# Kernel optimization log

Measured on AMD Instinct MI355X. Metric: run time of the kernel, lower is better.

The kernel has to match this reference:

```python
import jax, jax.numpy as jnp
import numpy as np

B, T, C, H = 4, 2048, 1024, 16
D = C // H  # head_dim = 64


def setup_inputs() -> dict:
    key = jax.random.key(0)
    k1, k2, k3, k4, k5 = jax.random.split(key, 5)
    x = jax.random.normal(k1, (B, T, C), dtype=jnp.float32)
    # torch nn.Linear weights: [out_features, in_features]
    s = 1.0 / np.sqrt(C)
    qkv_w = jax.random.uniform(k2, (3 * C, C), dtype=jnp.float32, minval=-s, maxval=s)
    qkv_b = jax.random.uniform(k3, (3 * C,), dtype=jnp.float32, minval=-s, maxval=s)
    out_w = jax.random.uniform(k4, (C, C), dtype=jnp.float32, minval=-s, maxval=s)
    out_b = jax.random.uniform(k5, (C,), dtype=jnp.float32, minval=-s, maxval=s)
    # causal mask broadcastable to [B,H,T,T]; 0 (False) marks masked positions
    attn_mask = jnp.tril(jnp.ones((T, T), dtype=bool))[None, None]
    return {"x": x, "qkv_w": qkv_w, "qkv_b": qkv_b, "out_w": out_w,
            "out_b": out_b, "attn_mask": attn_mask}


def reference(x, qkv_w, qkv_b, out_w, out_b, attn_mask):
    qkv = x @ qkv_w.T + qkv_b                      # [B,T,3C]
    q, k, v = jnp.split(qkv, 3, axis=-1)
    # [B,T,C] -> [B,H,T,D]
    q = q.reshape(B, T, H, D).transpose(0, 2, 1, 3)
    k = k.reshape(B, T, H, D).transpose(0, 2, 1, 3)
    v = v.reshape(B, T, H, D).transpose(0, 2, 1, 3)
    scale = 1.0 / np.sqrt(D)
    attn = jnp.einsum('bhqd,bhkd->bhqk', q, k) * scale   # [B,H,T,T]
    neg = jnp.finfo(attn.dtype).min
    attn = jnp.where(attn_mask, attn, neg)
    attn = jax.nn.softmax(attn, axis=-1)
    out = jnp.einsum('bhqk,bhkd->bhqd', attn, v)          # [B,H,T,D]
    out = out.transpose(0, 2, 1, 3).reshape(B, T, C)
    return out @ out_w.T + out_b
```

## Files before the change

kernel.cpp:

```cpp
#include <hip/hip_runtime.h>
#include <hip/hip_bf16.h>

#define B_ 4
#define T_ 2048
#define C_ 1024
#define H_ 16
#define D_ 64

typedef __hip_bfloat16 bf16;
typedef float f32x4 __attribute__((ext_vector_type(4)));
typedef short bf16s8 __attribute__((ext_vector_type(8)));

#define NEG_BIG (-1e30f)

__device__ inline unsigned short f2bf(float f) {
  __hip_bfloat16 h = __float2bfloat16(f);
  return *reinterpret_cast<unsigned short*>(&h);
}
__device__ inline float bf_lo(unsigned u) {
  union { unsigned u; float f; } c; c.u = u << 16; return c.f;
}

__device__ inline void async_load16(const void* g, void* l) {
  __builtin_amdgcn_global_load_lds(
      (const __attribute__((address_space(1))) unsigned int*)g,
      (__attribute__((address_space(3))) unsigned int*)l, 16, 0, 0);
}

union U4 { uint4 u; unsigned short s[8]; };

__device__ inline uint4 load8(const void* base, size_t idx, int f32) {
  if (f32) {
    const float* p = (const float*)base + idx;
    float4 a = *(const float4*)p;
    float4 b = *(const float4*)(p + 4);
    U4 r;
    r.s[0] = f2bf(a.x); r.s[1] = f2bf(a.y); r.s[2] = f2bf(a.z); r.s[3] = f2bf(a.w);
    r.s[4] = f2bf(b.x); r.s[5] = f2bf(b.y); r.s[6] = f2bf(b.z); r.s[7] = f2bf(b.w);
    return r.u;
  }
  return *(const uint4*)((const unsigned short*)base + idx);
}

__global__ void detect_k(const unsigned short* __restrict__ w, int* __restrict__ flag) {
  int lane = threadIdx.x;
  bool big = false;
  for (int i = lane; i < 512; i += 64) {
    float f = bf_lo((unsigned)w[i]);
    if (!(fabsf(f) <= 1.0f)) big = true;
  }
  int any = __any(big);
  if (lane == 0) *flag = any ? 1 : 0;
}

#define R_X   1048576
#define R_WQ  (R_X + 393216)
#define R_WO  (R_WQ + 131072)
#define R_BQ  (R_WO + 384)
#define R_BO  (R_BQ + 128)
__global__ __launch_bounds__(256) void convert_all_k(
    const void* __restrict__ x, const void* __restrict__ wq,
    const void* __restrict__ wo, const void* __restrict__ bq,
    const void* __restrict__ bo,
    bf16* __restrict__ xd, bf16* __restrict__ wqd, bf16* __restrict__ wod,
    bf16* __restrict__ bqd, bf16* __restrict__ bod,
    const int* __restrict__ flag) {
  const int f32 = *flag;
  long long g = (long long)blockIdx.x * 256 + threadIdx.x;
  if (g >= R_BO) return;
  const void* src; bf16* dst; long long base;
  if (g < R_X)       { src = x;  dst = xd;  base = 0; }
  else if (g < R_WQ) { src = wq; dst = wqd; base = R_X; }
  else if (g < R_WO) { src = wo; dst = wod; base = R_WQ; }
  else if (g < R_BQ) { src = bq; dst = bqd; base = R_WO; }
  else               { src = bo; dst = bod; base = R_BQ; }
  size_t i = (size_t)(g - base) * 8;
  *(uint4*)(dst + i) = load8(src, i, f32);
}

template <int KDIM, int MROWS>
__device__ inline void gemm_core(const bf16* __restrict__ A,
                                 const bf16* __restrict__ W,
                                 int tm, int tn, int wm, int wn,
                                 f32x4 acc[MROWS / 32][4], bf16* As, bf16* Bs) {
  const int tid  = threadIdx.x;
  const int lane = tid & 63;
  const int rl   = lane & 15;
  const int kq   = (lane >> 4) * 8;

  for (int k0 = 0; k0 < KDIM; k0 += 32) {
    __syncthreads();
#pragma unroll
    for (int j = 0; j < MROWS / 64; ++j) {
      int f    = j * 4096 + tid * 16;
      int row  = f >> 6;
      int colb = f & 63;
      async_load16((const char*)A + ((size_t)(tm + row) * KDIM + k0) * 2 + colb,
                   (char*)As + f);
    }
#pragma unroll
    for (int j = 0; j < 2; ++j) {
      int f    = j * 4096 + tid * 16;
      int row  = f >> 6;
      int colb = f & 63;
      async_load16((const char*)W + ((size_t)(tn + row) * KDIM + k0) * 2 + colb,
                   (char*)Bs + f);
    }
    __syncthreads();

    bf16s8 af[MROWS / 32], bw[4];
#pragma unroll
    for (int mt = 0; mt < MROWS / 32; ++mt)
      af[mt] = *(const bf16s8*)(As + (wm + mt * 16 + rl) * 32 + kq);
#pragma unroll
    for (int nt = 0; nt < 4; ++nt)
      bw[nt] = *(const bf16s8*)(Bs + (wn + nt * 16 + rl) * 32 + kq);

#pragma unroll
    for (int mt = 0; mt < MROWS / 32; ++mt)
#pragma unroll
      for (int nt = 0; nt < 4; ++nt)
        acc[mt][nt] = __builtin_amdgcn_mfma_f32_16x16x32_bf16(af[mt], bw[nt],
                                                              acc[mt][nt], 0, 0, 0);
  }
}

#define CSTRIDE 72
#define FSTRIDE 68

__global__ __launch_bounds__(256) void gemm_qkv_k(
    const bf16* __restrict__ X, const bf16* __restrict__ W,
    const bf16* __restrict__ bias,
    bf16* __restrict__ q, bf16* __restrict__ k, bf16* __restrict__ v) {
  __shared__ __align__(16) char smem[4 * 64 * CSTRIDE * 2];
  bf16* As = (bf16*)smem;
  bf16* Bs = (bf16*)(smem + 8192);
  const int tid = threadIdx.x;
  const int wave = tid >> 6, lane = tid & 63;
  const int tm = blockIdx.x * 128, tn = blockIdx.y * 128;
  const int wm = (wave >> 1) * 64, wn = (wave & 1) * 64;
  f32x4 acc[4][4];
#pragma unroll
  for (int i = 0; i < 4; ++i)
#pragma unroll
    for (int j = 0; j < 4; ++j) acc[i][j] = 0.0f;

  gemm_core<C_, 128>(X, W, tm, tn, wm, wn, acc, As, Bs);

  __syncthreads();
  bf16* Cs = (bf16*)smem + wave * 64 * CSTRIDE;

  const int rl = lane & 15, qd = lane >> 4;
  const int nbase = tn + wn;
  const int which = nbase >> 10;
  const int h = (nbase & 1023) >> 6;
  const float sc = which == 0 ? 0.125f : 1.0f;
  const int mbase = tm + wm;
  const int b = mbase >> 11, t0 = mbase & 2047;
  bf16* dst = which == 0 ? q : (which == 1 ? k : v);
  bf16* base = dst + (((size_t)(b * H_ + h)) * T_ + t0) * D_;

#pragma unroll
  for (int nt = 0; nt < 4; ++nt) {
    float bv = __bfloat162float(bias[nbase + nt * 16 + rl]);
#pragma unroll
    for (int mt = 0; mt < 4; ++mt)
#pragma unroll
      for (int r = 0; r < 4; ++r)
        Cs[(mt * 16 + qd * 4 + r) * CSTRIDE + nt * 16 + rl] =
            __float2bfloat16((acc[mt][nt][r] + bv) * sc);
  }
#pragma unroll
  for (int it = 0; it < 8; ++it) {
    int row = it * 8 + (lane >> 3);
    uint4 val = *(const uint4*)(Cs + row * CSTRIDE + (lane & 7) * 8);
    *(uint4*)(base + row * D_ + (lane & 7) * 8) = val;
  }
}

__global__ __launch_bounds__(256) void gemm_out_k(
    const bf16* __restrict__ O, const bf16* __restrict__ W,
    const bf16* __restrict__ bias, const int* __restrict__ flag,
    void* __restrict__ out) {
  __shared__ __align__(16) char smem[4 * 32 * FSTRIDE * 4];
  bf16* As = (bf16*)smem;
  bf16* Bs = (bf16*)(smem + 4096);
  const int f32 = *flag;
  const int tid = threadIdx.x;
  const int wave = tid >> 6, lane = tid & 63;
  const int tm = blockIdx.x * 64, tn = blockIdx.y * 128;
  const int wm = (wave >> 1) * 32, wn = (wave & 1) * 64;
  f32x4 acc[2][4];
#pragma unroll
  for (int i = 0; i < 2; ++i)
#pragma unroll
    for (int j = 0; j < 4; ++j) acc[i][j] = 0.0f;

  gemm_core<C_, 64>(O, W, tm, tn, wm, wn, acc, As, Bs);

  __syncthreads();
  const int rl = lane & 15, qd = lane >> 4;

  if (f32) {
    float* Cs = (float*)(smem + wave * 32 * FSTRIDE * 4);
#pragma unroll
    for (int nt = 0; nt < 4; ++nt) {
      float bv = __bfloat162float(bias[tn + wn + nt * 16 + rl]);
#pragma unroll
      for (int mt = 0; mt < 2; ++mt)
#pragma unroll
        for (int r = 0; r < 4; ++r)
          Cs[(mt * 16 + qd * 4 + r) * FSTRIDE + nt * 16 + rl] = acc[mt][nt][r] + bv;
    }
    float* obase = (float*)out + (size_t)(tm + wm) * C_ + tn + wn;
#pragma unroll
    for (int it = 0; it < 8; ++it) {
      int row = it * 4 + (lane >> 4);
      float4 val = *(const float4*)(Cs + row * FSTRIDE + (lane & 15) * 4);
      *(float4*)(obase + (size_t)row * C_ + (lane & 15) * 4) = val;
    }
  } else {
    bf16* Cs = (bf16*)(smem + wave * 32 * FSTRIDE * 4);
#pragma unroll
    for (int nt = 0; nt < 4; ++nt) {
      float bv = __bfloat162float(bias[tn + wn + nt * 16 + rl]);
#pragma unroll
      for (int mt = 0; mt < 2; ++mt)
#pragma unroll
        for (int r = 0; r < 4; ++r)
          Cs[(mt * 16 + qd * 4 + r) * CSTRIDE + nt * 16 + rl] =
              __float2bfloat16(acc[mt][nt][r] + bv);
    }
    bf16* obase = (bf16*)out + (size_t)(tm + wm) * C_ + tn + wn;
#pragma unroll
    for (int it = 0; it < 4; ++it) {
      int row = it * 8 + (lane >> 3);
      uint4 val = *(const uint4*)(Cs + row * CSTRIDE + (lane & 7) * 8);
      *(uint4*)(obase + (size_t)row * C_ + (lane & 7) * 8) = val;
    }
  }
}

#define PSTRIDE 72

__global__ __launch_bounds__(256) void fattn_k(
    const bf16* __restrict__ q, const bf16* __restrict__ k,
    const bf16* __restrict__ v, bf16* __restrict__ o) {
  __shared__ __align__(16) bf16 Ks[64 * 64];
  __shared__ __align__(16) bf16 Vs[64 * 64];
  __shared__ __align__(16) bf16 Ps[4 * 16 * PSTRIDE];
  const int tid = threadIdx.x, wave = tid >> 6, lane = tid & 63;
  const int rl = lane & 15, quad = lane >> 4;
  const int bh = blockIdx.x;
  const int b = bh >> 4, h = bh & 15;
  const size_t bhT = (size_t)bh * T_;
  bf16* Pw = Ps + wave * 16 * PSTRIDE;
  const int sw0 = (quad ^ (rl & 7)) << 3;
  const int sw1 = ((quad | 4) ^ (rl & 7)) << 3;

  bf16s8 ones;
#pragma unroll
  for (int i = 0; i < 8; ++i) ones[i] = (short)0x3F80;

  const int qb = 31 - blockIdx.y;
  const int q0 = qb * 64;

  const bf16* qr = q + (bhT + q0 + wave * 16 + rl) * D_;
  bf16s8 qf0 = *(const bf16s8*)(qr + quad * 8);
  bf16s8 qf1 = *(const bf16s8*)(qr + 32 + quad * 8);

  f32x4 oacc[4], lacc;
#pragma unroll
  for (int nt = 0; nt < 4; ++nt) oacc[nt] = 0.0f;
  lacc = 0.0f;

  const int nchunk = qb + 1;
#pragma unroll 1
  for (int c = 0; c < nchunk; ++c) {
    const int k0 = c << 6;
    __syncthreads();
#pragma unroll
    for (int r2 = 0; r2 < 2; ++r2) {
      int e = r2 * 2048 + tid * 8;
      int row = e >> 6;
      int cg  = (e >> 3) & 7;
      *(uint4*)(Ks + row * 64 + ((cg ^ (row & 7)) << 3)) =
          *(const uint4*)(k + (bhT + k0 + row) * D_ + cg * 8);
    }
    {
      int kp = tid & 31;
      int dg = tid >> 5;
      uint4 va = *(const uint4*)(v + (bhT + k0 + 2 * kp) * D_ + dg * 8);
      uint4 vb = *(const uint4*)(v + (bhT + k0 + 2 * kp + 1) * D_ + dg * 8);
      const unsigned* au = (const unsigned*)&va;
      const unsigned* bu = (const unsigned*)&vb;
#pragma unroll
      for (int m = 0; m < 4; ++m) {
        unsigned lo = (au[m] & 0xffffu) | (bu[m] << 16);
        unsigned hi = (au[m] >> 16) | (bu[m] & 0xffff0000u);
        int d0 = dg * 8 + 2 * m;
        int o0 = d0 * 64 + (((kp >> 2) ^ (2 * m)) << 3) + 2 * (kp & 3);
        int o1 = (d0 + 1) * 64 + (((kp >> 2) ^ (2 * m + 1)) << 3) + 2 * (kp & 3);
        *(unsigned*)(Vs + o0) = lo;
        *(unsigned*)(Vs + o1) = hi;
      }
    }
    __syncthreads();

    const int t0 = q0 + wave * 16;

    f32x4 s[4];
#pragma unroll
    for (int nt = 0; nt < 4; ++nt) s[nt] = 0.0f;
#pragma unroll
    for (int nt = 0; nt < 4; ++nt) {
      int key = nt * 16 + rl;
      bf16s8 kb0 = *(const bf16s8*)(Ks + key * 64 + sw0);
      bf16s8 kb1 = *(const bf16s8*)(Ks + key * 64 + sw1);
      s[nt] = __builtin_amdgcn_mfma_f32_16x16x32_bf16(qf0, kb0, s[nt], 0, 0, 0);
      s[nt] = __builtin_amdgcn_mfma_f32_16x16x32_bf16(qf1, kb1, s[nt], 0, 0, 0);
    }

    if (c == nchunk - 1) {
#pragma unroll
      for (int nt = 0; nt < 4; ++nt) {
        int key = k0 + nt * 16 + rl;
#pragma unroll
        for (int r = 0; r < 4; ++r) {
          int t = t0 + quad * 4 + r;
          if (key > t) s[nt][r] = NEG_BIG;
        }
      }
    }

#pragma unroll
    for (int nt = 0; nt < 4; ++nt)
#pragma unroll
      for (int r = 0; r < 4; ++r)
        s[nt][r] = __expf(fminf(s[nt][r], 30.0f));

#pragma unroll
    for (int nt = 0; nt < 4; ++nt)
#pragma unroll
      for (int r = 0; r < 4; ++r)
        Pw[(quad * 4 + r) * PSTRIDE + nt * 16 + rl] = __float2bfloat16(s[nt][r]);
    bf16s8 pa0 = *(const bf16s8*)(Pw + rl * PSTRIDE + quad * 8);
    bf16s8 pa1 = *(const bf16s8*)(Pw + rl * PSTRIDE + 32 + quad * 8);

    lacc = __builtin_amdgcn_mfma_f32_16x16x32_bf16(pa0, ones, lacc, 0, 0, 0);
    lacc = __builtin_amdgcn_mfma_f32_16x16x32_bf16(pa1, ones, lacc, 0, 0, 0);
#pragma unroll
    for (int nt = 0; nt < 4; ++nt) {
      int d = nt * 16 + rl;
      bf16s8 vb0 = *(const bf16s8*)(Vs + d * 64 + sw0);
      bf16s8 vb1 = *(const bf16s8*)(Vs + d * 64 + sw1);
      oacc[nt] = __builtin_amdgcn_mfma_f32_16x16x32_bf16(pa0, vb0, oacc[nt], 0, 0, 0);
      oacc[nt] = __builtin_amdgcn_mfma_f32_16x16x32_bf16(pa1, vb1, oacc[nt], 0, 0, 0);
    }
  }

  f32x4 linv;
#pragma unroll
  for (int r = 0; r < 4; ++r) linv[r] = 1.0f / lacc[r];
#pragma unroll
  for (int nt = 0; nt < 4; ++nt) {
    int d = nt * 16 + rl;
#pragma unroll
    for (int r = 0; r < 4; ++r) {
      int t = q0 + wave * 16 + quad * 4 + r;
      o[((size_t)b * T_ + t) * C_ + h * D_ + d] =
          __float2bfloat16(oacc[nt][r] * linv[r]);
    }
  }
}

extern "C" void kernel_launch(void* const* d_in, const int* in_sizes, int n_in,
                              void* d_out, int out_size, void* d_ws, size_t ws_size,
                              hipStream_t stream) {
  (void)in_sizes; (void)n_in; (void)out_size; (void)ws_size;
  const void* x     = d_in[0];
  const void* qkv_w = d_in[1];
  const void* qkv_b = d_in[2];
  const void* out_w = d_in[3];
  const void* out_b = d_in[4];

  const size_t nqkv = (size_t)B_ * T_ * C_;
  char* ws = (char*)d_ws;
  int*  flag = (int*)ws;
  bf16* q   = (bf16*)(ws + 256);
  bf16* kk  = q + nqkv;
  bf16* vv  = kk + nqkv;
  bf16* oo  = vv + nqkv;
  bf16* xbf = oo;
  bf16* wqkv = oo + nqkv;
  bf16* wout = wqkv + 3 * C_ * C_;
  bf16* bqkv = wout + C_ * C_;
  bf16* bout = bqkv + 3 * C_;

  detect_k<<<1, 64, 0, stream>>>((const unsigned short*)qkv_w, flag);
  convert_all_k<<<(R_BO + 255) / 256, 256, 0, stream>>>(
      x, qkv_w, out_w, qkv_b, out_b, xbf, wqkv, wout, bqkv, bout, flag);

  gemm_qkv_k<<<dim3(64, 24), 256, 0, stream>>>(xbf, wqkv, bqkv, q, kk, vv);
  fattn_k<<<dim3(64, 32), 256, 0, stream>>>(q, kk, vv, oo);
  gemm_out_k<<<dim3(128, 8), 256, 0, stream>>>(oo, wout, bout, flag, d_out);
}
```

Measured before the change: 271.9 us.

## Keep P in registers via transposed QK^T and permlane swaps; async-load K tile

The score MFMA swaps its operands so each lane holds S transposed (a query per lane, keys across registers). The softmax probabilities are then packed to bf16 and rearranged with permlane32/permlane16 swaps into the A-operand layout for the PV MFMA. This removes the per-wave LDS round trip for P. K tile loading now uses global_load_lds direct-to-LDS async copies instead of register-staged loads, which reduces VGPR traffic but relies on the builtin's lane-to-LDS address mapping matching the swizzle.

Result: no change. 273.2 us (+0.5%).

```diff
diff --git a/kernel.cpp b/kernel.cpp
--- a/kernel.cpp
+++ b/kernel.cpp
@@ -25,6 +25,15 @@
   __builtin_amdgcn_global_load_lds(
       (const __attribute__((address_space(1))) unsigned int*)g,
       (__attribute__((address_space(3))) unsigned int*)l, 16, 0, 0);
+}
+
+__device__ inline void plswap32(unsigned& a, unsigned& b) {
+  auto r = __builtin_amdgcn_permlane32_swap(a, b, false, false);
+  a = r[0]; b = r[1];
+}
+__device__ inline void plswap16(unsigned& a, unsigned& b) {
+  auto r = __builtin_amdgcn_permlane16_swap(a, b, false, false);
+  a = r[0]; b = r[1];
 }
 
 union U4 { uint4 u; unsigned short s[8]; };
@@ -241,20 +250,16 @@
   }
 }
 
-#define PSTRIDE 72
-
 __global__ __launch_bounds__(256) void fattn_k(
     const bf16* __restrict__ q, const bf16* __restrict__ k,
     const bf16* __restrict__ v, bf16* __restrict__ o) {
   __shared__ __align__(16) bf16 Ks[64 * 64];
   __shared__ __align__(16) bf16 Vs[64 * 64];
-  __shared__ __align__(16) bf16 Ps[4 * 16 * PSTRIDE];
   const int tid = threadIdx.x, wave = tid >> 6, lane = tid & 63;
   const int rl = lane & 15, quad = lane >> 4;
   const int bh = blockIdx.x;
   const int b = bh >> 4, h = bh & 15;
   const size_t bhT = (size_t)bh * T_;
-  bf16* Pw = Ps + wave * 16 * PSTRIDE;
   const int sw0 = (quad ^ (rl & 7)) << 3;
   const int sw1 = ((quad | 4) ^ (rl & 7)) << 3;
 
@@ -264,6 +269,11 @@
 
   const int qb = 31 - blockIdx.y;
   const int q0 = qb * 64;
+
+  const int kr0 = tid >> 3;
+  const int kc0 = ((tid & 7) ^ (kr0 & 7)) << 4;
+  const char* kstage = (const char*)k + (bhT + kr0) * (D_ * 2) + kc0;
+  char* kdst = (char*)Ks + tid * 16;
 
   const bf16* qr = q + (bhT + q0 + wave * 16 + rl) * D_;
   bf16s8 qf0 = *(const bf16s8*)(qr + quad * 8);
@@ -279,14 +289,8 @@
   for (int c = 0; c < nchunk; ++c) {
     const int k0 = c << 6;
     __syncthreads();
-#pragma unroll
-    for (int r2 = 0; r2 < 2; ++r2) {
-      int e = r2 * 2048 + tid * 8;
-      int row = e >> 6;
-      int cg  = (e >> 3) & 7;
-      *(uint4*)(Ks + row * 64 + ((cg ^ (row & 7)) << 3)) =
-          *(const uint4*)(k + (bhT + k0 + row) * D_ + cg * 8);
-    }
+    async_load16(kstage + (size_t)k0 * 128, kdst);
+    async_load16(kstage + (size_t)(k0 + 32) * 128, kdst + 4096);
     {
       int kp = tid & 31;
       int dg = tid >> 5;
@@ -317,35 +321,47 @@
       int key = nt * 16 + rl;
       bf16s8 kb0 = *(const bf16s8*)(Ks + key * 64 + sw0);
       bf16s8 kb1 = *(const bf16s8*)(Ks + key * 64 + sw1);
-      s[nt] = __builtin_amdgcn_mfma_f32_16x16x32_bf16(qf0, kb0, s[nt], 0, 0, 0);
-      s[nt] = __builtin_amdgcn_mfma_f32_16x16x32_bf16(qf1, kb1, s[nt], 0, 0, 0);
+      s[nt] = __builtin_amdgcn_mfma_f32_16x16x32_bf16(kb0, qf0, s[nt], 0, 0, 0);
+      s[nt] = __builtin_amdgcn_mfma_f32_16x16x32_bf16(kb1, qf1, s[nt], 0, 0, 0);
     }
 
     if (c == nchunk - 1) {
-#pragma unroll
-      for (int nt = 0; nt < 4; ++nt) {
-        int key = k0 + nt * 16 + rl;
+      int t = t0 + rl;
+#pragma unroll
+      for (int nt = 0; nt < 4; ++nt)
 #pragma unroll
         for (int r = 0; r < 4; ++r) {
-          int t = t0 + quad * 4 + r;
+          int key = k0 + nt * 16 + quad * 4 + r;
           if (key > t) s[nt][r] = NEG_BIG;
         }
-      }
-    }
-
-#pragma unroll
-    for (int nt = 0; nt < 4; ++nt)
+    }
+
+    unsigned pk[4][2];
+#pragma unroll
+    for (int nt = 0; nt < 4; ++nt) {
 #pragma unroll
       for (int r = 0; r < 4; ++r)
         s[nt][r] = __expf(fminf(s[nt][r], 30.0f));
-
-#pragma unroll
-    for (int nt = 0; nt < 4; ++nt)
-#pragma unroll
-      for (int r = 0; r < 4; ++r)
-        Pw[(quad * 4 + r) * PSTRIDE + nt * 16 + rl] = __float2bfloat16(s[nt][r]);
-    bf16s8 pa0 = *(const bf16s8*)(Pw + rl * PSTRIDE + quad * 8);
-    bf16s8 pa1 = *(const bf16s8*)(Pw + rl * PSTRIDE + 32 + quad * 8);
+      pk[nt][0] = (unsigned)f2bf(s[nt][0]) | ((unsigned)f2bf(s[nt][1]) << 16);
+      pk[nt][1] = (unsigned)f2bf(s[nt][2]) | ((unsigned)f2bf(s[nt][3]) << 16);
+    }
+
+    union { unsigned w[4]; bf16s8 v; } u0, u1;
+    {
+      unsigned a = pk[0][0], bq_ = pk[1][0];
+      plswap32(a, bq_); plswap16(a, bq_);
+      u0.w[0] = a; u0.w[2] = bq_;
+      a = pk[0][1]; bq_ = pk[1][1];
+      plswap32(a, bq_); plswap16(a, bq_);
+      u0.w[1] = a; u0.w[3] = bq_;
+      a = pk[2][0]; bq_ = pk[3][0];
+      plswap32(a, bq_); plswap16(a, bq_);
+      u1.w[0] = a; u1.w[2] = bq_;
+      a = pk[2][1]; bq_ = pk[3][1];
+      plswap32(a, bq_); plswap16(a, bq_);
+      u1.w[1] = a; u1.w[3] = bq_;
+    }
+    bf16s8 pa0 = u0.v, pa1 = u1.v;
 
     lacc = __builtin_amdgcn_mfma_f32_16x16x32_bf16(pa0, ones, lacc, 0, 0, 0);
     lacc = __builtin_amdgcn_mfma_f32_16x16x32_bf16(pa1, ones, lacc, 0, 0, 0);
```
